# Performance work log

Hardware: AMD Instinct MI355X
Metric: run time of the kernel (lower is better)

## Reference

```python
import jax, jax.numpy as jnp
from jax import lax
import numpy as np

B, T, F, U = 256, 512, 32, 350


def setup_inputs() -> dict:
    key = jax.random.key(0)
    ks = jax.random.split(key, 5)
    # Glorot-normal-ish scales for weights
    kernel = jax.random.normal(ks[0], (F, 4 * U), jnp.float32) * np.sqrt(2.0 / (F + 4 * U))
    recurrent_kernel = jax.random.normal(ks[1], (U, 4 * U), jnp.float32) * np.sqrt(2.0 / (U + 4 * U))
    dense_w = jax.random.normal(ks[2], (U, 1), jnp.float32) * np.sqrt(2.0 / (U + 1))
    return {
        "x": jax.random.normal(ks[3], (B, T, F), jnp.float32),
        "kernel": kernel,
        "recurrent_kernel": recurrent_kernel,
        "bias": jnp.zeros((4 * U,), jnp.float32),
        "dense_w": dense_w,
        "dense_b": jnp.zeros((1,), jnp.float32),
    }


def reference(x, kernel, recurrent_kernel, bias, dense_w, dense_b):
    # Keras LSTM with activation='relu' (candidate + cell-output activation),
    # recurrent_activation=sigmoid (default). Gate order: i, f, c, o.
    b, t, f = x.shape
    u = recurrent_kernel.shape[0]
    # Precompute input projection for all timesteps: [B, T, 4U]
    xz = jnp.einsum('btf,fg->btg', x, kernel) + bias

    def step(carry, xt):
        h, c = carry
        z = xt + h @ recurrent_kernel  # [B, 4U]
        zi, zf, zg, zo = jnp.split(z, 4, axis=-1)
        i = jax.nn.sigmoid(zi)
        fg = jax.nn.sigmoid(zf)
        g = jax.nn.relu(zg)          # activation='relu' on candidate
        o = jax.nn.sigmoid(zo)
        c_new = fg * c + i * g
        h_new = o * jax.nn.relu(c_new)  # activation='relu' on output
        return (h_new, c_new), h_new

    h0 = jnp.zeros((b, u), x.dtype)
    c0 = jnp.zeros((b, u), x.dtype)
    (_, _), hs = lax.scan(step, (h0, c0), jnp.swapaxes(xz, 0, 1))  # hs: [T, B, U]
    hs = jnp.swapaxes(hs, 0, 1)  # [B, T, U] (return_sequences=True)
    return hs @ dense_w + dense_b  # [B, T, 1]
```

## Files before the change

### kernel.cpp

```cpp
#include <hip/hip_runtime.h>
#include <stdint.h>


#define T_   512
#define F_   32
#define U_   350
#define G4   1400
#define NGRP 16
#define NB   16
#define NCB  11
#define KC   12
#define NT   88
#define HSLOTUS 5632
#define SLOTW   5632

typedef __attribute__((ext_vector_type(8))) short  short8;
typedef __attribute__((ext_vector_type(4))) short  short4_;
typedef __attribute__((ext_vector_type(4))) float  float4_;
typedef unsigned long long u64t;

__device__ __forceinline__ short f2bf(float f) {
  union { float f; uint32_t u; } v; v.f = f;
  return (short)((v.u + 0x7FFFu + ((v.u >> 16) & 1u)) >> 16);
}

#define SZ_W     (NT*KC*64*8*2u)
#define OFF_XBF  (SZ_W)
#define SZ_XBF   (256u*T_*F_*2u)
#define OFF_HBUF (OFF_XBF + SZ_XBF)
#define SZ_HBUF  (NGRP*2u*HSLOTUS*2u)
#define OFF_HMIR (OFF_HBUF + SZ_HBUF)
#define SZ_HMIR  (NGRP*2u*SLOTW*4u)
#define OFF_TAG  (OFF_HMIR + SZ_HMIR)
#define SZ_TAG   (NGRP*2u*32u*4u)
#define OFF_FLG  (OFF_TAG + SZ_TAG)
#define SZ_FLG   (NGRP*16u*4u)
#define OFF_WP   (OFF_FLG + SZ_FLG)
#define SZ_WP    (NGRP*NCB*NB*T_*4u)

__global__ void prep_w(const float* __restrict__ kern,
                       const float* __restrict__ rk,
                       const float* __restrict__ bias,
                       short* __restrict__ wswz) {
  const int tile = blockIdx.x, lane = threadIdx.x;
  const int g = tile / 22, jt = tile % 22;
  const int colg = jt * 16 + (lane & 15);
  const int src = g * U_ + colg;
  const bool valid = (colg < U_);
  const int kbase = (lane >> 4) * 8;
  for (int kc = 0; kc < KC; ++kc) {
    short8 pack;
    #pragma unroll
    for (int jj = 0; jj < 8; ++jj) {
      int k = kc * 32 + kbase + jj;
      float v = 0.f;
      if (valid) {
        if (k < F_)            v = kern[k * G4 + src];
        else if (k < F_ + U_)  v = rk[(k - F_) * G4 + src];
        else if (k == F_ + U_) v = bias[src];
      }
      pack[jj] = f2bf(v);
    }
    *(short8*)(wswz + (((size_t)kc * NT + tile) * 64 + lane) * 8) = pack;
  }
}

__global__ void prep_x(const float* __restrict__ x, short* __restrict__ xbf) {
  int i = (blockIdx.x * 256 + threadIdx.x) * 4;
  float4_ v = *(const float4_*)(x + i);
  short4_ o;
  #pragma unroll
  for (int jj = 0; jj < 4; ++jj) o[jj] = f2bf(v[jj]);
  *(short4_*)(xbf + i) = o;
}

__global__ void init_all(unsigned short* __restrict__ hb16,
                         uint32_t* __restrict__ hmir32,
                         uint32_t* __restrict__ tagbuf,
                         uint32_t* __restrict__ flagbuf) {
  int i = blockIdx.x * 256 + threadIdx.x;
  int grp = i / HSLOTUS, rem = i % HSLOTUS;
  {
    int blk = rem >> 9, quadc = (rem >> 7) & 3, cpos = rem & 7;
    int col = blk * 32 + quadc * 8 + cpos;
    hb16[(size_t)(grp * 2 + 1) * HSLOTUS + rem] =
        (col == 350) ? (unsigned short)0x3F80 : 0;
  }
  {
    int blkm = rem >> 8, off = rem & 255;
    int fi = blkm >> 1, fk2 = blkm & 1, fquadc = off >> 6;
    int fk1 = (off >> 1) & 1, fb = off & 1;
    int fcol = fi * 32 + fquadc * 8 + fk2 * 4 + fk1 * 2 + fb;
    hmir32[(size_t)(grp * 2 + 1) * SLOTW + rem] =
        (fcol == 350) ? 0x3F800000u : 0u;
  }
  if (rem < 32) {
    tagbuf[(size_t)(grp * 2 + 0) * 32 + rem] = 0u;
    tagbuf[(size_t)(grp * 2 + 1) * 32 + rem] = 0u;
  }
  if (rem == 0) flagbuf[grp * 16] = 0u;
}

__global__ __launch_bounds__(128)
__attribute__((amdgpu_waves_per_eu(1, 1)))
void lstm_kernel(const short* __restrict__ xbf, const short* __restrict__ wswz,
                 unsigned short* __restrict__ hb16, uint32_t* __restrict__ hmir32,
                 uint32_t* __restrict__ tagbuf, uint32_t* __restrict__ flagbuf,
                 const float* __restrict__ dense_w, float* __restrict__ wpart) {
  __shared__ float lds_part[2][T_][16];

  const int tid  = threadIdx.x;
  const int lane = tid & 63;
  const int wv   = tid >> 6;
  const int l15  = lane & 15;
  const int quad = lane >> 4;
  const int grp  = blockIdx.x & 15;
  const int j    = blockIdx.x >> 4;
  const int tileg = 2 * j + wv;

  short8 wreg[4][KC];
  #pragma unroll
  for (int g = 0; g < 4; ++g)
    #pragma unroll
    for (int kc = 0; kc < KC; ++kc)
      wreg[g][kc] = *(const short8*)(wswz +
          (((size_t)kc * NT + (g * 22 + tileg)) * 64 + lane) * 8);

  const int col = tileg * 16 + l15;
  const float dwv = (col < U_) ? dense_w[col] : 0.f;
  float cst[4] = {0.f, 0.f, 0.f, 0.f};

  const int pblk = col >> 5, pc32 = col & 31;
  const int pbase_us = pblk * 512 + ((pc32 >> 3) * 16 + quad * 4) * 8 + (pc32 & 7);
  const int colrem = col & 31;
  const int fastoff = (((col >> 5) * 2 + ((colrem >> 2) & 1)) * 256)
                    + (((colrem >> 3) * 16 + quad * 4) * 4)
                    + (((colrem >> 1) & 1) * 2) + (col & 1);

  const short* xrow = xbf + ((size_t)(grp * NB + l15) * T_) * F_ + quad * 8;
  unsigned short* hbb = hb16 + (size_t)grp * 2 * HSLOTUS;
  uint32_t* hm  = hmir32 + (size_t)grp * 2 * SLOTW;
  uint32_t* tgg = tagbuf + (size_t)grp * 2 * 32;
  uint32_t* flagp = flagbuf + grp * 16;
  const int tagidx = (lane < 22) ? lane : 31;

  bool mm = false;
  const short hs_init = (col == 350) ? (short)0x3F80 : 0;
  uint32_t wout[4], wout_prev[4];
  #pragma unroll
  for (int r = 0; r < 4; ++r)
    wout[r] = wout_prev[r] = ((uint32_t)(unsigned short)hs_init) << 16;

  #pragma unroll 1
  for (int t = 0; t < T_; ++t) {
    short8 axf = *(const short8*)(xrow + t * F_);

    const uint32_t want = (uint32_t)t;
    const uint32_t* tgr = tgg + (size_t)((t + 1) & 1) * 32;
    uint32_t tv = __hip_atomic_load(tgr + tagidx, __ATOMIC_RELAXED,
                                    __HIP_MEMORY_SCOPE_AGENT);

    float4_ acc[4];
    #pragma unroll
    for (int g = 0; g < 4; ++g) {
      float4_ z = (float4_){0.f, 0.f, 0.f, 0.f};
      acc[g] = __builtin_amdgcn_mfma_f32_16x16x32_bf16(axf, wreg[g][0], z, 0, 0, 0);
    }

    short8 afr[11];
    bool ready = (bool)__all((int)(lane >= 22 || tv == want));
    bool gotm = false;
    int tries = 0;
    while (!ready) {
      ++tries;
      if (!mm) {
        if ((tries & 63) == 0) {
          uint32_t f = __hip_atomic_load(flagp, __ATOMIC_RELAXED,
                                         __HIP_MEMORY_SCOPE_SYSTEM);
          if (f) mm = true;
        }
        if (tries == 16384) {
          if (lane == 0)
            __hip_atomic_store(flagp, 1u, __ATOMIC_RELAXED,
                               __HIP_MEMORY_SCOPE_SYSTEM);
          mm = true;
        }
        if (mm) {
          uint32_t* md1 = hm + (size_t)((t + 1) & 1) * SLOTW + fastoff;
          uint32_t* md0 = hm + (size_t)(t & 1) * SLOTW + fastoff;
          #pragma unroll
          for (int r = 0; r < 4; ++r) {
            __hip_atomic_store(md1 + r * 4, wout[r], __ATOMIC_RELAXED,
                               __HIP_MEMORY_SCOPE_AGENT);
            __hip_atomic_store(md0 + r * 4, wout_prev[r], __ATOMIC_RELAXED,
                               __HIP_MEMORY_SCOPE_AGENT);
          }
        }
      } else {
        const u64t* mq = (const u64t*)(hm + (size_t)((t + 1) & 1) * SLOTW)
                       + (size_t)lane * 2;
        u64t q[44];
        #pragma unroll
        for (int i = 0; i < 11; ++i) {
          const u64t* pa = mq + (size_t)(2 * i) * 128;
          const u64t* pb = mq + (size_t)(2 * i + 1) * 128;
          q[4 * i + 0] = __hip_atomic_load(pa,     __ATOMIC_RELAXED, __HIP_MEMORY_SCOPE_AGENT);
          q[4 * i + 1] = __hip_atomic_load(pa + 1, __ATOMIC_RELAXED, __HIP_MEMORY_SCOPE_AGENT);
          q[4 * i + 2] = __hip_atomic_load(pb,     __ATOMIC_RELAXED, __HIP_MEMORY_SCOPE_AGENT);
          q[4 * i + 3] = __hip_atomic_load(pb + 1, __ATOMIC_RELAXED, __HIP_MEMORY_SCOPE_AGENT);
        }
        const uint32_t tag16 = want & 0xFFFFu;
        uint32_t bad = 0;
        #pragma unroll
        for (int i = 0; i < 44; ++i) {
          bad |= ((uint32_t)q[i] ^ tag16);
          bad |= ((uint32_t)(q[i] >> 32) ^ tag16);
        }
        if ((bool)__all((int)((bad & 0xFFFFu) == 0))) {
          #pragma unroll
          for (int i = 0; i < 11; ++i) {
            union { uint32_t w[4]; short8 s; } u;
            #pragma unroll
            for (int k = 0; k < 4; ++k) {
              uint32_t lo = (uint32_t)q[4 * i + k];
              uint32_t hi = (uint32_t)(q[4 * i + k] >> 32);
              u.w[k] = (lo >> 16) | (hi & 0xFFFF0000u);
            }
            afr[i] = u.s;
          }
          gotm = true;
          break;
        }
      }
      tv = __hip_atomic_load(tgr + tagidx, __ATOMIC_RELAXED,
                             __HIP_MEMORY_SCOPE_AGENT);
      ready = (bool)__all((int)(lane >= 22 || tv == want));
    }

    if (!gotm) {
      const u64t* hq = (const u64t*)(hbb + (size_t)((t + 1) & 1) * HSLOTUS)
                     + (size_t)lane * 2;
      #pragma unroll
      for (int i = 0; i < 11; ++i) {
        union { u64t q[2]; short8 s; } u;
        u.q[0] = __hip_atomic_load(hq + (size_t)i * 128,     __ATOMIC_RELAXED, __HIP_MEMORY_SCOPE_AGENT);
        u.q[1] = __hip_atomic_load(hq + (size_t)i * 128 + 1, __ATOMIC_RELAXED, __HIP_MEMORY_SCOPE_AGENT);
        afr[i] = u.s;
      }
    }

    #pragma unroll
    for (int i = 0; i < 11; ++i)
      #pragma unroll
      for (int g = 0; g < 4; ++g)
        acc[g] = __builtin_amdgcn_mfma_f32_16x16x32_bf16(afr[i], wreg[g][i + 1], acc[g], 0, 0, 0);

    unsigned short* hwp = hbb + (size_t)(t & 1) * HSLOTUS + pbase_us;
    const uint32_t otag = (uint32_t)(t + 1);
    float hn[4];
    #pragma unroll
    for (int r = 0; r < 4; ++r) {
      float ig = __builtin_amdgcn_rcpf(1.f + __expf(-acc[0][r]));
      float fg = __builtin_amdgcn_rcpf(1.f + __expf(-acc[1][r]));
      float gg = fmaxf(acc[2][r], 0.f);
      float og = __builtin_amdgcn_rcpf(1.f + __expf(-acc[3][r]));
      float cn = fg * cst[r] + ig * gg;
      cst[r] = cn;
      hn[r] = og * fmaxf(cn, 0.f);
      short hs = f2bf(hn[r]);
      if (col == 350) hs = (short)0x3F80;
      else if (col == 351) hs = 0;
      wout_prev[r] = wout[r];
      wout[r] = (((uint32_t)(unsigned short)hs) << 16) | (otag & 0xFFFFu);
      hwp[r * 8] = (unsigned short)hs;
    }
    if (lane == 0)
      __hip_atomic_store(tgg + (size_t)(t & 1) * 32 + tileg, otag,
                         __ATOMIC_RELEASE, __HIP_MEMORY_SCOPE_WORKGROUP);
    if (mm) {
      uint32_t* hwrm = hm + (size_t)(t & 1) * SLOTW + fastoff;
      #pragma unroll
      for (int r = 0; r < 4; ++r)
        __hip_atomic_store(hwrm + r * 4, wout[r], __ATOMIC_RELAXED,
                           __HIP_MEMORY_SCOPE_AGENT);
    }

    #pragma unroll
    for (int r = 0; r < 4; ++r) {
      float s = hn[r] * dwv;
      s += __shfl_xor(s, 1); s += __shfl_xor(s, 2);
      s += __shfl_xor(s, 4); s += __shfl_xor(s, 8);
      if (l15 == 0) lds_part[wv][t][quad * 4 + r] = s;
    }
  }

  __syncthreads();
  float* wp = wpart + ((size_t)(grp * NCB + j) * NB) * T_;
  for (int i = tid; i < NB * T_; i += 128) {
    int t = i & (T_ - 1), row = i >> 9;
    wp[(size_t)row * T_ + t] = lds_part[0][t][row] + lds_part[1][t][row];
  }
}

__global__ void reduce_out(const float* __restrict__ wpart,
                           const float* __restrict__ dense_b,
                           float* __restrict__ out) {
  int i = blockIdx.x * 256 + threadIdx.x;
  int b = i >> 9, t = i & 511;
  int grp = b >> 4, row = b & 15;
  float s = dense_b[0];
  #pragma unroll
  for (int j = 0; j < NCB; ++j)
    s += wpart[(((size_t)grp * NCB + j) * NB + row) * T_ + t];
  out[i] = s;
}

extern "C" void kernel_launch(void* const* d_in, const int* in_sizes, int n_in,
                              void* d_out, int out_size, void* d_ws, size_t ws_size,
                              hipStream_t stream) {
  const float* x    = (const float*)d_in[0];
  const float* kern = (const float*)d_in[1];
  const float* rk   = (const float*)d_in[2];
  const float* bias = (const float*)d_in[3];
  const float* dw   = (const float*)d_in[4];
  const float* db   = (const float*)d_in[5];
  float* out = (float*)d_out;

  char* ws = (char*)d_ws;
  short*          wswz   = (short*)(ws);
  short*          xbf    = (short*)(ws + OFF_XBF);
  unsigned short* hb16   = (unsigned short*)(ws + OFF_HBUF);
  uint32_t*       hmir32 = (uint32_t*)(ws + OFF_HMIR);
  uint32_t*       tagbuf = (uint32_t*)(ws + OFF_TAG);
  uint32_t*       flagbuf= (uint32_t*)(ws + OFF_FLG);
  float*          wpart  = (float*)(ws + OFF_WP);

  prep_w<<<NT, 64, 0, stream>>>(kern, rk, bias, wswz);
  prep_x<<<(256 * T_ * F_) / (256 * 4), 256, 0, stream>>>(x, xbf);
  init_all<<<(NGRP * HSLOTUS) / 256, 256, 0, stream>>>(hb16, hmir32, tagbuf, flagbuf);
  lstm_kernel<<<NGRP * NCB, 128, 0, stream>>>(xbf, wswz, hb16, hmir32, tagbuf,
                                              flagbuf, dw, wpart);
  reduce_out<<<(256 * T_) / 256, 256, 0, stream>>>(wpart, db, out);
}
```

Before: 1.000 ms.

## Use tagged 32-bit hidden-state words so loads self-validate, speculating past tag waits

The primary hidden-state buffer now stores each bf16 value with a 16-bit step tag in a 32-bit word, the same format as the mirror buffer. Consumers load the previous step's state and run the recurrent MFMAs at once, then check the embedded tags and retry if any are stale. The tag-flag wait is kept but is no longer needed for correctness, so its store is relaxed from release, and the dense-output shuffle reduction is deferred one step to overlap the loads. In exchange, hidden-state memory traffic doubles and the MFMA work is thrown away and redone whenever a load sees stale data.

```diff
diff --git a/kernel.cpp b/kernel.cpp
--- a/kernel.cpp
+++ b/kernel.cpp
@@ -11,8 +11,7 @@
 #define NCB  11
 #define KC   12
 #define NT   88
-#define HSLOTUS 5632
-#define SLOTW   5632
+#define SLOTW 5632
 
 typedef __attribute__((ext_vector_type(8))) short  short8;
 typedef __attribute__((ext_vector_type(4))) short  short4_;
@@ -28,7 +27,7 @@
 #define OFF_XBF  (SZ_W)
 #define SZ_XBF   (256u*T_*F_*2u)
 #define OFF_HBUF (OFF_XBF + SZ_XBF)
-#define SZ_HBUF  (NGRP*2u*HSLOTUS*2u)
+#define SZ_HBUF  (NGRP*2u*SLOTW*4u)
 #define OFF_HMIR (OFF_HBUF + SZ_HBUF)
 #define SZ_HMIR  (NGRP*2u*SLOTW*4u)
 #define OFF_TAG  (OFF_HMIR + SZ_HMIR)
@@ -74,37 +73,43 @@
   *(short4_*)(xbf + i) = o;
 }
 
-__global__ void init_all(unsigned short* __restrict__ hb16,
+__global__ void init_all(uint32_t* __restrict__ hbuf32,
                          uint32_t* __restrict__ hmir32,
                          uint32_t* __restrict__ tagbuf,
                          uint32_t* __restrict__ flagbuf) {
   int i = blockIdx.x * 256 + threadIdx.x;
-  int grp = i / HSLOTUS, rem = i % HSLOTUS;
-  {
-    int blk = rem >> 9, quadc = (rem >> 7) & 3, cpos = rem & 7;
-    int col = blk * 32 + quadc * 8 + cpos;
-    hb16[(size_t)(grp * 2 + 1) * HSLOTUS + rem] =
-        (col == 350) ? (unsigned short)0x3F80 : 0;
-  }
-  {
-    int blkm = rem >> 8, off = rem & 255;
-    int fi = blkm >> 1, fk2 = blkm & 1, fquadc = off >> 6;
-    int fk1 = (off >> 1) & 1, fb = off & 1;
-    int fcol = fi * 32 + fquadc * 8 + fk2 * 4 + fk1 * 2 + fb;
-    hmir32[(size_t)(grp * 2 + 1) * SLOTW + rem] =
-        (fcol == 350) ? 0x3F800000u : 0u;
-  }
+  int grp = i / SLOTW, rem = i % SLOTW;
+  int blk = rem >> 8, off = rem & 255;
+  int fi = blk >> 1, fk2 = blk & 1, fquadc = off >> 6;
+  int fk1 = (off >> 1) & 1, fb = off & 1;
+  int fcol = fi * 32 + fquadc * 8 + fk2 * 4 + fk1 * 2 + fb;
+  uint32_t v = (fcol == 350) ? 0x3F800000u : 0u;
+  size_t idx = (size_t)(grp * 2 + 1) * SLOTW + rem;
+  hbuf32[idx] = v;
+  hmir32[idx] = v;
   if (rem < 32) {
     tagbuf[(size_t)(grp * 2 + 0) * 32 + rem] = 0u;
     tagbuf[(size_t)(grp * 2 + 1) * 32 + rem] = 0u;
   }
-  if (rem == 0) flagbuf[grp * 16] = 0u;
+  if (rem == 32) flagbuf[grp * 16] = 0u;
+}
+
+__device__ __forceinline__ void loadq44(u64t* q, const u64t* dq) {
+  #pragma unroll
+  for (int i = 0; i < 11; ++i) {
+    const u64t* pa = dq + (size_t)(2 * i) * 128;
+    const u64t* pb = dq + (size_t)(2 * i + 1) * 128;
+    q[4 * i + 0] = __hip_atomic_load(pa,     __ATOMIC_RELAXED, __HIP_MEMORY_SCOPE_AGENT);
+    q[4 * i + 1] = __hip_atomic_load(pa + 1, __ATOMIC_RELAXED, __HIP_MEMORY_SCOPE_AGENT);
+    q[4 * i + 2] = __hip_atomic_load(pb,     __ATOMIC_RELAXED, __HIP_MEMORY_SCOPE_AGENT);
+    q[4 * i + 3] = __hip_atomic_load(pb + 1, __ATOMIC_RELAXED, __HIP_MEMORY_SCOPE_AGENT);
+  }
 }
 
 __global__ __launch_bounds__(128)
 __attribute__((amdgpu_waves_per_eu(1, 1)))
 void lstm_kernel(const short* __restrict__ xbf, const short* __restrict__ wswz,
-                 unsigned short* __restrict__ hb16, uint32_t* __restrict__ hmir32,
+                 uint32_t* __restrict__ hbuf32, uint32_t* __restrict__ hmir32,
                  uint32_t* __restrict__ tagbuf, uint32_t* __restrict__ flagbuf,
                  const float* __restrict__ dense_w, float* __restrict__ wpart) {
   __shared__ float lds_part[2][T_][16];
@@ -130,15 +135,13 @@
   const float dwv = (col < U_) ? dense_w[col] : 0.f;
   float cst[4] = {0.f, 0.f, 0.f, 0.f};
 
-  const int pblk = col >> 5, pc32 = col & 31;
-  const int pbase_us = pblk * 512 + ((pc32 >> 3) * 16 + quad * 4) * 8 + (pc32 & 7);
   const int colrem = col & 31;
   const int fastoff = (((col >> 5) * 2 + ((colrem >> 2) & 1)) * 256)
                     + (((colrem >> 3) * 16 + quad * 4) * 4)
                     + (((colrem >> 1) & 1) * 2) + (col & 1);
 
   const short* xrow = xbf + ((size_t)(grp * NB + l15) * T_) * F_ + quad * 8;
-  unsigned short* hbb = hb16 + (size_t)grp * 2 * HSLOTUS;
+  uint32_t* hb  = hbuf32 + (size_t)grp * 2 * SLOTW;
   uint32_t* hm  = hmir32 + (size_t)grp * 2 * SLOTW;
   uint32_t* tgg = tagbuf + (size_t)grp * 2 * 32;
   uint32_t* flagp = flagbuf + grp * 16;
@@ -150,6 +153,7 @@
   #pragma unroll
   for (int r = 0; r < 4; ++r)
     wout[r] = wout_prev[r] = ((uint32_t)(unsigned short)hs_init) << 16;
+  float hn_prev[4] = {0.f, 0.f, 0.f, 0.f};
 
   #pragma unroll 1
   for (int t = 0; t < T_; ++t) {
@@ -160,20 +164,18 @@
     uint32_t tv = __hip_atomic_load(tgr + tagidx, __ATOMIC_RELAXED,
                                     __HIP_MEMORY_SCOPE_AGENT);
 
-    float4_ acc[4];
+    float4_ acc0[4];
     #pragma unroll
     for (int g = 0; g < 4; ++g) {
       float4_ z = (float4_){0.f, 0.f, 0.f, 0.f};
-      acc[g] = __builtin_amdgcn_mfma_f32_16x16x32_bf16(axf, wreg[g][0], z, 0, 0, 0);
-    }
-
-    short8 afr[11];
-    bool ready = (bool)__all((int)(lane >= 22 || tv == want));
-    bool gotm = false;
-    int tries = 0;
-    while (!ready) {
-      ++tries;
-      if (!mm) {
+      acc0[g] = __builtin_amdgcn_mfma_f32_16x16x32_bf16(axf, wreg[g][0], z, 0, 0, 0);
+    }
+
+    if (!mm) {
+      bool ready = (bool)__all((int)(lane >= 22 || tv == want));
+      int tries = 0;
+      while (!ready) {
+        ++tries;
         if ((tries & 63) == 0) {
           uint32_t f = __hip_atomic_load(flagp, __ATOMIC_RELAXED,
                                          __HIP_MEMORY_SCOPE_SYSTEM);
@@ -195,69 +197,74 @@
             __hip_atomic_store(md0 + r * 4, wout_prev[r], __ATOMIC_RELAXED,
                                __HIP_MEMORY_SCOPE_AGENT);
           }
-        }
-      } else {
-        const u64t* mq = (const u64t*)(hm + (size_t)((t + 1) & 1) * SLOTW)
-                       + (size_t)lane * 2;
-        u64t q[44];
-        #pragma unroll
-        for (int i = 0; i < 11; ++i) {
-          const u64t* pa = mq + (size_t)(2 * i) * 128;
-          const u64t* pb = mq + (size_t)(2 * i + 1) * 128;
-          q[4 * i + 0] = __hip_atomic_load(pa,     __ATOMIC_RELAXED, __HIP_MEMORY_SCOPE_AGENT);
-          q[4 * i + 1] = __hip_atomic_load(pa + 1, __ATOMIC_RELAXED, __HIP_MEMORY_SCOPE_AGENT);
-          q[4 * i + 2] = __hip_atomic_load(pb,     __ATOMIC_RELAXED, __HIP_MEMORY_SCOPE_AGENT);
-          q[4 * i + 3] = __hip_atomic_load(pb + 1, __ATOMIC_RELAXED, __HIP_MEMORY_SCOPE_AGENT);
-        }
-        const uint32_t tag16 = want & 0xFFFFu;
-        uint32_t bad = 0;
-        #pragma unroll
-        for (int i = 0; i < 44; ++i) {
-          bad |= ((uint32_t)q[i] ^ tag16);
-          bad |= ((uint32_t)(q[i] >> 32) ^ tag16);
-        }
-        if ((bool)__all((int)((bad & 0xFFFFu) == 0))) {
-          #pragma unroll
-          for (int i = 0; i < 11; ++i) {
-            union { uint32_t w[4]; short8 s; } u;
-            #pragma unroll
-            for (int k = 0; k < 4; ++k) {
-              uint32_t lo = (uint32_t)q[4 * i + k];
-              uint32_t hi = (uint32_t)(q[4 * i + k] >> 32);
-              u.w[k] = (lo >> 16) | (hi & 0xFFFF0000u);
-            }
-            afr[i] = u.s;
-          }
-          gotm = true;
           break;
         }
-      }
-      tv = __hip_atomic_load(tgr + tagidx, __ATOMIC_RELAXED,
-                             __HIP_MEMORY_SCOPE_AGENT);
-      ready = (bool)__all((int)(lane >= 22 || tv == want));
-    }
-
-    if (!gotm) {
-      const u64t* hq = (const u64t*)(hbb + (size_t)((t + 1) & 1) * HSLOTUS)
-                     + (size_t)lane * 2;
+        tv = __hip_atomic_load(tgr + tagidx, __ATOMIC_RELAXED,
+                               __HIP_MEMORY_SCOPE_AGENT);
+        ready = (bool)__all((int)(lane >= 22 || tv == want));
+      }
+    }
+
+    u64t q[44];
+    {
+      const u64t* dq = (const u64t*)((mm ? hm : hb)
+                       + (size_t)((t + 1) & 1) * SLOTW) + (size_t)lane * 2;
+      loadq44(q, dq);
+    }
+    if (t) {
+      #pragma unroll
+      for (int r = 0; r < 4; ++r) {
+        float s = hn_prev[r];
+        s += __shfl_xor(s, 1); s += __shfl_xor(s, 2);
+        s += __shfl_xor(s, 4); s += __shfl_xor(s, 8);
+        if (l15 == 0) lds_part[wv][t - 1][quad * 4 + r] = s;
+      }
+    }
+
+    const u64t tp = (u64t)(want & 0xFFFFu) * 0x0000000100000001ull;
+    float4_ acc[4];
+    int vtries = 0;
+    for (;;) {
+      u64t bad = 0;
       #pragma unroll
       for (int i = 0; i < 11; ++i) {
-        union { u64t q[2]; short8 s; } u;
-        u.q[0] = __hip_atomic_load(hq + (size_t)i * 128,     __ATOMIC_RELAXED, __HIP_MEMORY_SCOPE_AGENT);
-        u.q[1] = __hip_atomic_load(hq + (size_t)i * 128 + 1, __ATOMIC_RELAXED, __HIP_MEMORY_SCOPE_AGENT);
-        afr[i] = u.s;
-      }
-    }
-
-    #pragma unroll
-    for (int i = 0; i < 11; ++i)
-      #pragma unroll
-      for (int g = 0; g < 4; ++g)
-        acc[g] = __builtin_amdgcn_mfma_f32_16x16x32_bf16(afr[i], wreg[g][i + 1], acc[g], 0, 0, 0);
-
-    unsigned short* hwp = hbb + (size_t)(t & 1) * HSLOTUS + pbase_us;
+        union { uint32_t w[4]; short8 s; } u;
+        #pragma unroll
+        for (int k = 0; k < 4; ++k) {
+          uint32_t lo = (uint32_t)q[4 * i + k];
+          uint32_t hi = (uint32_t)(q[4 * i + k] >> 32);
+          u.w[k] = (lo >> 16) | (hi & 0xFFFF0000u);
+          bad |= (q[4 * i + k] ^ tp);
+        }
+        #pragma unroll
+        for (int g = 0; g < 4; ++g)
+          acc[g] = __builtin_amdgcn_mfma_f32_16x16x32_bf16(
+              u.s, wreg[g][i + 1], (i == 0) ? acc0[g] : acc[g], 0, 0, 0);
+      }
+      bad &= 0x0000FFFF0000FFFFull;
+      if ((bool)__all((int)(bad == 0))) break;
+      if (!mm && ++vtries >= 4096) {
+        if (lane == 0)
+          __hip_atomic_store(flagp, 1u, __ATOMIC_RELAXED,
+                             __HIP_MEMORY_SCOPE_SYSTEM);
+        mm = true;
+        uint32_t* md1 = hm + (size_t)((t + 1) & 1) * SLOTW + fastoff;
+        uint32_t* md0 = hm + (size_t)(t & 1) * SLOTW + fastoff;
+        #pragma unroll
+        for (int r = 0; r < 4; ++r) {
+          __hip_atomic_store(md1 + r * 4, wout[r], __ATOMIC_RELAXED,
+                             __HIP_MEMORY_SCOPE_AGENT);
+          __hip_atomic_store(md0 + r * 4, wout_prev[r], __ATOMIC_RELAXED,
+                             __HIP_MEMORY_SCOPE_AGENT);
+        }
+      }
+      const u64t* dq = (const u64t*)((mm ? hm : hb)
+                       + (size_t)((t + 1) & 1) * SLOTW) + (size_t)lane * 2;
+      loadq44(q, dq);
+    }
+
+    uint32_t* hwr = hb + (size_t)(t & 1) * SLOTW;
     const uint32_t otag = (uint32_t)(t + 1);
-    float hn[4];
     #pragma unroll
     for (int r = 0; r < 4; ++r) {
       float ig = __builtin_amdgcn_rcpf(1.f + __expf(-acc[0][r]));
@@ -266,17 +273,19 @@
       float og = __builtin_amdgcn_rcpf(1.f + __expf(-acc[3][r]));
       float cn = fg * cst[r] + ig * gg;
       cst[r] = cn;
-      hn[r] = og * fmaxf(cn, 0.f);
-      short hs = f2bf(hn[r]);
+      float hnr = og * fmaxf(cn, 0.f);
+      hn_prev[r] = hnr * dwv;
+      short hs = f2bf(hnr);
       if (col == 350) hs = (short)0x3F80;
       else if (col == 351) hs = 0;
       wout_prev[r] = wout[r];
       wout[r] = (((uint32_t)(unsigned short)hs) << 16) | (otag & 0xFFFFu);
-      hwp[r * 8] = (unsigned short)hs;
+      __hip_atomic_store(hwr + fastoff + r * 4, wout[r],
+                         __ATOMIC_RELAXED, __HIP_MEMORY_SCOPE_WORKGROUP);
     }
     if (lane == 0)
       __hip_atomic_store(tgg + (size_t)(t & 1) * 32 + tileg, otag,
-                         __ATOMIC_RELEASE, __HIP_MEMORY_SCOPE_WORKGROUP);
+                         __ATOMIC_RELAXED, __HIP_MEMORY_SCOPE_WORKGROUP);
     if (mm) {
       uint32_t* hwrm = hm + (size_t)(t & 1) * SLOTW + fastoff;
       #pragma unroll
@@ -284,14 +293,14 @@
         __hip_atomic_store(hwrm + r * 4, wout[r], __ATOMIC_RELAXED,
                            __HIP_MEMORY_SCOPE_AGENT);
     }
-
-    #pragma unroll
-    for (int r = 0; r < 4; ++r) {
-      float s = hn[r] * dwv;
-      s += __shfl_xor(s, 1); s += __shfl_xor(s, 2);
-      s += __shfl_xor(s, 4); s += __shfl_xor(s, 8);
-      if (l15 == 0) lds_part[wv][t][quad * 4 + r] = s;
-    }
+  }
+
+  #pragma unroll
+  for (int r = 0; r < 4; ++r) {
+    float s = hn_prev[r];
+    s += __shfl_xor(s, 1); s += __shfl_xor(s, 2);
+    s += __shfl_xor(s, 4); s += __shfl_xor(s, 8);
+    if (l15 == 0) lds_part[wv][T_ - 1][quad * 4 + r] = s;
   }
 
   __syncthreads();
@@ -327,18 +336,18 @@
   float* out = (float*)d_out;
 
   char* ws = (char*)d_ws;
-  short*          wswz   = (short*)(ws);
-  short*          xbf    = (short*)(ws + OFF_XBF);
-  unsigned short* hb16   = (unsigned short*)(ws + OFF_HBUF);
-  uint32_t*       hmir32 = (uint32_t*)(ws + OFF_HMIR);
-  uint32_t*       tagbuf = (uint32_t*)(ws + OFF_TAG);
-  uint32_t*       flagbuf= (uint32_t*)(ws + OFF_FLG);
-  float*          wpart  = (float*)(ws + OFF_WP);
+  short*    wswz   = (short*)(ws);
+  short*    xbf    = (short*)(ws + OFF_XBF);
+  uint32_t* hbuf32 = (uint32_t*)(ws + OFF_HBUF);
+  uint32_t* hmir32 = (uint32_t*)(ws + OFF_HMIR);
+  uint32_t* tagbuf = (uint32_t*)(ws + OFF_TAG);
+  uint32_t* flagbuf= (uint32_t*)(ws + OFF_FLG);
+  float*    wpart  = (float*)(ws + OFF_WP);
 
   prep_w<<<NT, 64, 0, stream>>>(kern, rk, bias, wswz);
   prep_x<<<(256 * T_ * F_) / (256 * 4), 256, 0, stream>>>(x, xbf);
-  init_all<<<(NGRP * HSLOTUS) / 256, 256, 0, stream>>>(hb16, hmir32, tagbuf, flagbuf);
-  lstm_kernel<<<NGRP * NCB, 128, 0, stream>>>(xbf, wswz, hb16, hmir32, tagbuf,
+  init_all<<<(NGRP * SLOTW) / 256, 256, 0, stream>>>(hbuf32, hmir32, tagbuf, flagbuf);
+  lstm_kernel<<<NGRP * NCB, 128, 0, stream>>>(xbf, wswz, hbuf32, hmir32, tagbuf,
                                               flagbuf, dw, wpart);
   reduce_out<<<(256 * T_) / 256, 256, 0, stream>>>(wpart, db, out);
 }
```

Result: slower. 1.372 ms (+37.2%).
